# Performance work log

Measured on AMD Instinct MI355X. Metric: run time of the kernel, lower is better.

The kernel has to match this reference:

```python
import jax, jax.numpy as jnp
import numpy as np

B, T, D = 1, 1024, 1024
H, KVH, HD = 16, 4, 64          # heads, kv heads, head dim (D = H*HD)
E, K, FF = 8, 2, 2048           # experts, top_k, expert hidden
CF, ROPE_THETA, CLIP = 2.0, 500000.0, 8.0
CAP = int(np.ceil(B * T * K * CF / E))  # per-expert capacity (=512)
EPS = 1e-5


def layernorm(x, w):
    mu = jnp.mean(x, -1, keepdims=True)
    var = jnp.var(x, -1, keepdims=True)
    return (x - mu) * jax.lax.rsqrt(var + EPS) * w


def rotate_half(u):
    u1, u2 = u[..., : HD // 2], u[..., HD // 2 :]
    return jnp.concatenate([-u2, u1], axis=-1)


def rope(q, k, position_ids):
    inv_freq = 1.0 / (ROPE_THETA ** (jnp.arange(0, HD, 2, dtype=jnp.float32) / HD))
    ang = position_ids.astype(jnp.float32)[..., None] * inv_freq  # (B,T,HD/2)
    emb = jnp.concatenate([ang, ang], axis=-1)                    # (B,T,HD)
    cos = jnp.cos(emb)[:, :, None, :]  # broadcast over heads -> (B,T,1,HD)
    sin = jnp.sin(emb)[:, :, None, :]
    q = q * cos + rotate_half(q) * sin
    k = k * cos + rotate_half(k) * sin
    return q, k


def setup_inputs() -> dict:
    key = jax.random.key(0)
    ks = jax.random.split(key, 12)
    s = 0.02
    return {
        "hidden_states": jax.random.normal(ks[0], (B, T, D), jnp.float32),
        "position_ids": jnp.tile(jnp.arange(T, dtype=jnp.int32)[None, :], (B, 1)),
        "ln1_w": jnp.ones((D,), jnp.float32),
        "ln2_w": jnp.ones((D,), jnp.float32),
        "Wq": jax.random.normal(ks[1], (D, H * HD), jnp.float32) * s,
        "Wk": jax.random.normal(ks[2], (D, KVH * HD), jnp.float32) * s,
        "Wv": jax.random.normal(ks[3], (D, KVH * HD), jnp.float32) * s,
        "Wo": jax.random.normal(ks[4], (H * HD, D), jnp.float32) * s,
        "Wr": jax.random.normal(ks[5], (D, E), jnp.float32) * s,
        "Wg": jax.random.normal(ks[6], (E, D, FF), jnp.float32) * s,
        "Wu": jax.random.normal(ks[7], (E, D, FF), jnp.float32) * s,
        "Wd": jax.random.normal(ks[8], (E, FF, D), jnp.float32) * s,
    }


def reference(hidden_states, position_ids, ln1_w, ln2_w, Wq, Wk, Wv, Wo, Wr, Wg, Wu, Wd):
    x = hidden_states
    # ---- attention (pre-LN, clip_qkv, RoPE, GQA, causal) ----
    res = x
    h = layernorm(x, ln1_w)
    q = jnp.clip(h @ Wq, -CLIP, CLIP).reshape(B, T, H, HD)
    k = jnp.clip(h @ Wk, -CLIP, CLIP).reshape(B, T, KVH, HD)
    v = jnp.clip(h @ Wv, -CLIP, CLIP).reshape(B, T, KVH, HD)
    q, k = rope(q, k, position_ids)
    k = jnp.repeat(k, H // KVH, axis=2)  # GQA expand -> (B,T,H,HD)
    v = jnp.repeat(v, H // KVH, axis=2)
    scores = jnp.einsum("bthd,bshd->bhts", q, k) / jnp.sqrt(jnp.float32(HD))
    causal = jnp.tril(jnp.ones((T, T), bool))
    scores = jnp.where(causal[None, None], scores, jnp.finfo(scores.dtype).min)
    attn = jax.nn.softmax(scores, axis=-1)
    o = jnp.einsum("bhts,bshd->bthd", attn, v).reshape(B, T, H * HD) @ Wo
    x = res + o
    # ---- MoE FFN (top-k router, capacity-based dispatch, GLU experts) ----
    res = x
    h = layernorm(x, ln2_w).reshape(B * T, D)
    N = B * T
    probs = jax.nn.softmax(h @ Wr, axis=-1)            # (N,E)
    vals, idx = jax.lax.top_k(probs, K)                # (N,K)
    gate = vals / jnp.sum(vals, -1, keepdims=True)     # normalize_top_k_affinities
    e_flat = idx.reshape(-1)                           # (N*K,)
    g_flat = gate.reshape(-1)
    tok = jnp.repeat(jnp.arange(N), K)                 # source token per assignment
    oh = jax.nn.one_hot(e_flat, E, dtype=jnp.int32)
    pos = jnp.cumsum(oh, axis=0)[jnp.arange(N * K), e_flat] - 1  # slot within expert
    keep = pos < CAP                                   # capacity drop mask
    slot = jnp.where(keep, pos, CAP)                   # overflow -> trash slot
    xb = jnp.zeros((E, CAP + 1, D), h.dtype).at[e_flat, slot].set(h[tok])
    act = jax.nn.silu(jnp.einsum("ecd,edf->ecf", xb, Wg)) * jnp.einsum("ecd,edf->ecf", xb, Wu)
    ob = jnp.einsum("ecf,efd->ecd", act, Wd)           # (E,CAP+1,D)
    contrib = ob[e_flat, slot] * (g_flat * keep.astype(h.dtype))[:, None]
    y = jnp.zeros((N, D), h.dtype).at[tok].add(contrib).reshape(B, T, D)
    return res + y
```

## Files before the change

kernel.cpp:

```cpp
#include <hip/hip_runtime.h>
#include <math.h>

typedef __attribute__((ext_vector_type(8))) short bfrag;
typedef __attribute__((ext_vector_type(8))) unsigned short u16x8;
typedef __attribute__((ext_vector_type(4))) float f32x4;

__device__ __forceinline__ unsigned short bf16_rne(float f) {
  unsigned int u = __float_as_uint(f);
  u += 0x7FFFu + ((u >> 16) & 1u);
  return (unsigned short)(u >> 16);
}
__device__ __forceinline__ float bf16f(unsigned short h) {
  return __uint_as_float(((unsigned int)h) << 16);
}
__device__ __forceinline__ void split3(float x, unsigned short &o1, unsigned short &o2, unsigned short &o3) {
  o1 = bf16_rne(x);
  const float r1 = x - bf16f(o1);
  o2 = bf16_rne(r1);
  const float r2 = r1 - bf16f(o2);
  o3 = bf16_rne(r2);
}
__device__ __forceinline__ void split2(float x, unsigned short &o1, unsigned short &o2) {
  o1 = bf16_rne(x);
  o2 = bf16_rne(x - bf16f(o1));
}

__global__ __launch_bounds__(256) void ln_kernel(const float* __restrict__ x,
                                                 const float* __restrict__ w,
                                                 float* __restrict__ out) {
  const int t = blockIdx.x;
  const int tid = threadIdx.x;
  const float4 v = *reinterpret_cast<const float4*>(&x[(size_t)t * 1024 + tid * 4]);
  float s = v.x + v.y + v.z + v.w;
  float ss = v.x * v.x + v.y * v.y + v.z * v.z + v.w * v.w;
#pragma unroll
  for (int off = 32; off; off >>= 1) {
    s += __shfl_xor(s, off);
    ss += __shfl_xor(ss, off);
  }
  __shared__ float red1[4], red2[4];
  if ((tid & 63) == 0) { red1[tid >> 6] = s; red2[tid >> 6] = ss; }
  __syncthreads();
  s = red1[0] + red1[1] + red1[2] + red1[3];
  ss = red2[0] + red2[1] + red2[2] + red2[3];
  const float mu = s * (1.0f / 1024.0f);
  const float var = ss * (1.0f / 1024.0f) - mu * mu;
  const float rstd = 1.0f / sqrtf(var + 1e-5f);
  const float4 wv = *reinterpret_cast<const float4*>(&w[tid * 4]);
  float4 o;
  o.x = (v.x - mu) * rstd * wv.x;
  o.y = (v.y - mu) * rstd * wv.y;
  o.z = (v.z - mu) * rstd * wv.z;
  o.w = (v.w - mu) * rstd * wv.w;
  *reinterpret_cast<float4*>(&out[(size_t)t * 1024 + tid * 4]) = o;
}

__global__ __launch_bounds__(256) void ln_split3_kernel(
    const float* __restrict__ x, const float* __restrict__ w,
    unsigned short* __restrict__ d1, unsigned short* __restrict__ d2,
    unsigned short* __restrict__ d3) {
  const int t = blockIdx.x;
  const int tid = threadIdx.x;
  const float4 v = *reinterpret_cast<const float4*>(&x[(size_t)t * 1024 + tid * 4]);
  float s = v.x + v.y + v.z + v.w;
  float ss = v.x * v.x + v.y * v.y + v.z * v.z + v.w * v.w;
#pragma unroll
  for (int off = 32; off; off >>= 1) {
    s += __shfl_xor(s, off);
    ss += __shfl_xor(ss, off);
  }
  __shared__ float red1[4], red2[4];
  if ((tid & 63) == 0) { red1[tid >> 6] = s; red2[tid >> 6] = ss; }
  __syncthreads();
  s = red1[0] + red1[1] + red1[2] + red1[3];
  ss = red2[0] + red2[1] + red2[2] + red2[3];
  const float mu = s * (1.0f / 1024.0f);
  const float var = ss * (1.0f / 1024.0f) - mu * mu;
  const float rstd = 1.0f / sqrtf(var + 1e-5f);
  const float4 wv = *reinterpret_cast<const float4*>(&w[tid * 4]);
  float4 o;
  o.x = (v.x - mu) * rstd * wv.x;
  o.y = (v.y - mu) * rstd * wv.y;
  o.z = (v.z - mu) * rstd * wv.z;
  o.w = (v.w - mu) * rstd * wv.w;
  ushort4 a, b, c;
  split3(o.x, a.x, b.x, c.x);
  split3(o.y, a.y, b.y, c.y);
  split3(o.z, a.z, b.z, c.z);
  split3(o.w, a.w, b.w, c.w);
  const int i = t * 256 + tid;
  reinterpret_cast<ushort4*>(d1)[i] = a;
  reinterpret_cast<ushort4*>(d2)[i] = b;
  reinterpret_cast<ushort4*>(d3)[i] = c;
}

__global__ __launch_bounds__(256) void split3t_kernel(
    const float* __restrict__ src, unsigned short* __restrict__ d1,
    unsigned short* __restrict__ d2, unsigned short* __restrict__ d3,
    int K, int N) {
  __shared__ float tile[32][33];
  const int k0 = blockIdx.x * 32, n0 = blockIdx.y * 32;
  const int tx = threadIdx.x & 31, ty = threadIdx.x >> 5;
#pragma unroll
  for (int i = 0; i < 4; ++i)
    tile[ty + i * 8][tx] = src[(size_t)(k0 + ty + i * 8) * N + n0 + tx];
  __syncthreads();
#pragma unroll
  for (int i = 0; i < 4; ++i) {
    const float v = tile[tx][ty + i * 8];
    unsigned short s1, s2, s3;
    split3(v, s1, s2, s3);
    const size_t o = (size_t)(n0 + ty + i * 8) * K + k0 + tx;
    d1[o] = s1; d2[o] = s2; d3[o] = s3;
  }
}

__device__ __forceinline__ void gemm_ps_body(
    const unsigned short* __restrict__ A1, const unsigned short* __restrict__ A2,
    const unsigned short* __restrict__ A3, const unsigned short* __restrict__ B1,
    const unsigned short* __restrict__ B2, const unsigned short* __restrict__ B3,
    float* __restrict__ C, const float* __restrict__ Res,
    int N, int K, int doclip, int m0, int n0) {
  __shared__ alignas(16) unsigned short As[3][32][40];
  __shared__ alignas(16) unsigned short Bs[3][64][40];
  const int tid = threadIdx.x;
  const int w = tid >> 6, l = tid & 63;
  const int wm = (w & 1) * 16, wn = (w >> 1) * 32;
  const int lr = l & 15, lg = l >> 4;
  const int arow = tid >> 3, aslot = tid & 7;

  const unsigned short* Ap[3] = {A1, A2, A3};
  const unsigned short* Bp[3] = {B1, B2, B3};

  f32x4 acc[2] = {{0.f,0.f,0.f,0.f},{0.f,0.f,0.f,0.f}};

  for (int k0 = 0; k0 < K; k0 += 32) {
#pragma unroll
    for (int s = 0; s < 3; ++s) {
      *reinterpret_cast<ushort4*>(&As[s][arow][aslot * 4]) =
          *reinterpret_cast<const ushort4*>(&Ap[s][(size_t)(m0 + arow) * K + k0 + aslot * 4]);
#pragma unroll
      for (int p = 0; p < 2; ++p) {
        const int row = arow + p * 32;
        *reinterpret_cast<ushort4*>(&Bs[s][row][aslot * 4]) =
            *reinterpret_cast<const ushort4*>(&Bp[s][(size_t)(n0 + row) * K + k0 + aslot * 4]);
      }
    }
    __syncthreads();
    bfrag af[3], bg[2][3];
#pragma unroll
    for (int s = 0; s < 3; ++s)
      af[s] = *reinterpret_cast<const bfrag*>(&As[s][wm + lr][lg * 8]);
#pragma unroll
    for (int ni = 0; ni < 2; ++ni)
#pragma unroll
      for (int s = 0; s < 3; ++s)
        bg[ni][s] = *reinterpret_cast<const bfrag*>(&Bs[s][wn + ni * 16 + lr][lg * 8]);
#pragma unroll
    for (int ni = 0; ni < 2; ++ni) {
      f32x4 c = acc[ni];
      c = __builtin_amdgcn_mfma_f32_16x16x32_bf16(af[2], bg[ni][0], c, 0, 0, 0);
      c = __builtin_amdgcn_mfma_f32_16x16x32_bf16(af[1], bg[ni][1], c, 0, 0, 0);
      c = __builtin_amdgcn_mfma_f32_16x16x32_bf16(af[0], bg[ni][2], c, 0, 0, 0);
      c = __builtin_amdgcn_mfma_f32_16x16x32_bf16(af[1], bg[ni][0], c, 0, 0, 0);
      c = __builtin_amdgcn_mfma_f32_16x16x32_bf16(af[0], bg[ni][1], c, 0, 0, 0);
      c = __builtin_amdgcn_mfma_f32_16x16x32_bf16(af[0], bg[ni][0], c, 0, 0, 0);
      acc[ni] = c;
    }
    __syncthreads();
  }
#pragma unroll
  for (int ni = 0; ni < 2; ++ni)
#pragma unroll
    for (int r = 0; r < 4; ++r) {
      const int row = m0 + wm + lg * 4 + r;
      const int col = n0 + wn + ni * 16 + lr;
      float vv = acc[ni][r];
      if (doclip) vv = fminf(fmaxf(vv, -8.0f), 8.0f);
      if (Res) vv += Res[(size_t)row * N + col];
      C[(size_t)row * N + col] = vv;
    }
}

__global__ __launch_bounds__(256) void gemm_ps_kernel(
    const unsigned short* __restrict__ A1, const unsigned short* __restrict__ A2,
    const unsigned short* __restrict__ A3, const unsigned short* __restrict__ B1,
    const unsigned short* __restrict__ B2, const unsigned short* __restrict__ B3,
    float* __restrict__ C, const float* __restrict__ Res,
    int N, int K, int doclip) {
  gemm_ps_body(A1, A2, A3, B1, B2, B3, C, Res, N, K, doclip,
               blockIdx.x * 32, blockIdx.y * 64);
}

__global__ __launch_bounds__(256) void gemm_qkv_kernel(
    const unsigned short* __restrict__ A1, const unsigned short* __restrict__ A2,
    const unsigned short* __restrict__ A3,
    const unsigned short* __restrict__ Q1, const unsigned short* __restrict__ Q2,
    const unsigned short* __restrict__ Q3,
    const unsigned short* __restrict__ K1, const unsigned short* __restrict__ K2,
    const unsigned short* __restrict__ K3,
    const unsigned short* __restrict__ V1, const unsigned short* __restrict__ V2,
    const unsigned short* __restrict__ V3,
    float* __restrict__ qb, float* __restrict__ kb, float* __restrict__ vb) {
  const int by = blockIdx.y;
  const unsigned short *B1, *B2, *B3;
  float* C;
  int N, n0;
  if (by < 16)      { B1 = Q1; B2 = Q2; B3 = Q3; C = qb; N = 1024; n0 = by * 64; }
  else if (by < 20) { B1 = K1; B2 = K2; B3 = K3; C = kb; N = 256;  n0 = (by - 16) * 64; }
  else              { B1 = V1; B2 = V2; B3 = V3; C = vb; N = 256;  n0 = (by - 20) * 64; }
  gemm_ps_body(A1, A2, A3, B1, B2, B3, C, nullptr, N, 1024, 1, blockIdx.x * 32, n0);
}

__global__ void rope_table_kernel(const int* __restrict__ posids,
                                  float* __restrict__ cosT, float* __restrict__ sinT) {
  const int t = blockIdx.x * 8 + (threadIdx.x >> 5);
  const int i = threadIdx.x & 31;
  const double ang = (double)posids[t] * pow(500000.0, -(double)i / 32.0);
  cosT[t * 32 + i] = (float)cos(ang);
  sinT[t * 32 + i] = (float)sin(ang);
}

__global__ void rope_kernel(float* __restrict__ q, float* __restrict__ k,
                            const float* __restrict__ cosT, const float* __restrict__ sinT) {
  const int t = blockIdx.x;
  const int hh = blockIdx.y;
  const int i = threadIdx.x;
  float* ptr = (hh < 16) ? &q[((size_t)t * 16 + hh) * 64]
                         : &k[((size_t)t * 4 + (hh - 16)) * 64];
  const float c = cosT[t * 32 + i], s = sinT[t * 32 + i];
  const float u1 = ptr[i], u2 = ptr[i + 32];
  ptr[i]      = u1 * c - u2 * s;
  ptr[i + 32] = u2 * c + u1 * s;
}

__global__ __launch_bounds__(256) void prep_kv_kernel(
    const float* __restrict__ k, const float* __restrict__ v,
    unsigned short* __restrict__ Kp1, unsigned short* __restrict__ Kp2,
    unsigned short* __restrict__ Vp1, unsigned short* __restrict__ Vp2) {
  const int key = blockIdx.x;
  const int kvh = threadIdx.x >> 6;
  const int d = threadIdx.x & 63;
  const float kk = k[((size_t)key * 4 + kvh) * 64 + d];
  const float vv = v[((size_t)key * 4 + kvh) * 64 + d];
  unsigned short a1, a2, b1, b2;
  split2(kk, a1, a2);
  split2(vv, b1, b2);
  const size_t ki = ((size_t)kvh * 1024 + key) * 64 + d;
  Kp1[ki] = a1; Kp2[ki] = a2;
  const size_t vi = ((size_t)kvh * 64 + d) * 1024 + key;
  Vp1[vi] = b1; Vp2[vi] = b2;
}

__global__ __launch_bounds__(256) void attn_kernel(
    const float* __restrict__ q,
    const unsigned short* __restrict__ Kp1, const unsigned short* __restrict__ Kp2,
    const unsigned short* __restrict__ Vp1, const unsigned short* __restrict__ Vp2,
    unsigned short* __restrict__ o1, unsigned short* __restrict__ o2,
    unsigned short* __restrict__ o3) {
  const int qt = blockIdx.x, h = blockIdx.y, kvh = h >> 2;
  __shared__ unsigned short Ks1[64][72], Ks2[64][72], Vt1[64][72], Vt2[64][72];
  __shared__ unsigned short Ps1[4][16][72], Ps2[4][16][72];
  const int tid = threadIdx.x;
  const int w = tid >> 6, l = tid & 63;
  const int lr = l & 15, lg = l >> 4;

  bfrag aq1[2], aq2[2];
  {
    const int tq = qt * 64 + w * 16 + lr;
    const float* qrow = &q[((size_t)tq * 16 + h) * 64];
#pragma unroll
    for (int ks = 0; ks < 2; ++ks) {
      const int d0 = ks * 32 + lg * 8;
      const float4 f0 = *reinterpret_cast<const float4*>(qrow + d0);
      const float4 f1 = *reinterpret_cast<const float4*>(qrow + d0 + 4);
      const float xv[8] = {f0.x, f0.y, f0.z, f0.w, f1.x, f1.y, f1.z, f1.w};
#pragma unroll
      for (int j = 0; j < 8; ++j) {
        const float xs = xv[j] * 0.125f;
        unsigned short p1, p2;
        split2(xs, p1, p2);
        aq1[ks][j] = (short)p1;
        aq2[ks][j] = (short)p2;
      }
    }
  }

  f32x4 accO[4] = {{0.f,0.f,0.f,0.f},{0.f,0.f,0.f,0.f},{0.f,0.f,0.f,0.f},{0.f,0.f,0.f,0.f}};
  float mrun[4] = {-INFINITY, -INFINITY, -INFINITY, -INFINITY};
  float lrun[4] = {0.f, 0.f, 0.f, 0.f};

  for (int ti = 0; ti <= qt; ++ti) {
    const int s0 = ti * 64;
    {
      const size_t kbase = ((size_t)kvh * 1024 + s0 + l) * 64 + w * 16;
      *reinterpret_cast<u16x8*>(&Ks1[l][w * 16])     = *reinterpret_cast<const u16x8*>(&Kp1[kbase]);
      *reinterpret_cast<u16x8*>(&Ks1[l][w * 16 + 8]) = *reinterpret_cast<const u16x8*>(&Kp1[kbase + 8]);
      *reinterpret_cast<u16x8*>(&Ks2[l][w * 16])     = *reinterpret_cast<const u16x8*>(&Kp2[kbase]);
      *reinterpret_cast<u16x8*>(&Ks2[l][w * 16 + 8]) = *reinterpret_cast<const u16x8*>(&Kp2[kbase + 8]);
      const size_t vbase = ((size_t)kvh * 64 + l) * 1024 + s0 + w * 16;
      *reinterpret_cast<u16x8*>(&Vt1[l][w * 16])     = *reinterpret_cast<const u16x8*>(&Vp1[vbase]);
      *reinterpret_cast<u16x8*>(&Vt1[l][w * 16 + 8]) = *reinterpret_cast<const u16x8*>(&Vp1[vbase + 8]);
      *reinterpret_cast<u16x8*>(&Vt2[l][w * 16])     = *reinterpret_cast<const u16x8*>(&Vp2[vbase]);
      *reinterpret_cast<u16x8*>(&Vt2[l][w * 16 + 8]) = *reinterpret_cast<const u16x8*>(&Vp2[vbase + 8]);
    }
    __syncthreads();

    f32x4 accS[4] = {{0.f,0.f,0.f,0.f},{0.f,0.f,0.f,0.f},{0.f,0.f,0.f,0.f},{0.f,0.f,0.f,0.f}};
#pragma unroll
    for (int ks = 0; ks < 2; ++ks) {
      const int koff = ks * 32 + lg * 8;
#pragma unroll
      for (int ni = 0; ni < 4; ++ni) {
        const bfrag b1 = *reinterpret_cast<const bfrag*>(&Ks1[ni * 16 + lr][koff]);
        const bfrag b2 = *reinterpret_cast<const bfrag*>(&Ks2[ni * 16 + lr][koff]);
        f32x4 c = accS[ni];
        c = __builtin_amdgcn_mfma_f32_16x16x32_bf16(aq1[ks], b2, c, 0, 0, 0);
        c = __builtin_amdgcn_mfma_f32_16x16x32_bf16(aq2[ks], b1, c, 0, 0, 0);
        c = __builtin_amdgcn_mfma_f32_16x16x32_bf16(aq1[ks], b1, c, 0, 0, 0);
        accS[ni] = c;
      }
    }
    if (ti == qt) {
      const int rowb = w * 16 + lg * 4;
#pragma unroll
      for (int ni = 0; ni < 4; ++ni)
#pragma unroll
        for (int r = 0; r < 4; ++r)
          if (ni * 16 + lr > rowb + r) accS[ni][r] = -INFINITY;
    }
    float alpha[4];
#pragma unroll
    for (int r = 0; r < 4; ++r) {
      float tm = fmaxf(fmaxf(accS[0][r], accS[1][r]), fmaxf(accS[2][r], accS[3][r]));
      tm = fmaxf(tm, __shfl_xor(tm, 1));
      tm = fmaxf(tm, __shfl_xor(tm, 2));
      tm = fmaxf(tm, __shfl_xor(tm, 4));
      tm = fmaxf(tm, __shfl_xor(tm, 8));
      const float mnew = fmaxf(mrun[r], tm);
      alpha[r] = __expf(mrun[r] - mnew);
      mrun[r] = mnew;
      float ps = 0.f;
#pragma unroll
      for (int ni = 0; ni < 4; ++ni) {
        const float pv = __expf(accS[ni][r] - mnew);
        accS[ni][r] = pv;
        ps += pv;
      }
      ps += __shfl_xor(ps, 1);
      ps += __shfl_xor(ps, 2);
      ps += __shfl_xor(ps, 4);
      ps += __shfl_xor(ps, 8);
      lrun[r] = lrun[r] * alpha[r] + ps;
    }
#pragma unroll
    for (int ni = 0; ni < 4; ++ni)
#pragma unroll
      for (int r = 0; r < 4; ++r) {
        const float pv = accS[ni][r];
        unsigned short p1, p2;
        split2(pv, p1, p2);
        Ps1[w][lg * 4 + r][ni * 16 + lr] = p1;
        Ps2[w][lg * 4 + r][ni * 16 + lr] = p2;
      }
#pragma unroll
    for (int ni = 0; ni < 4; ++ni)
#pragma unroll
      for (int r = 0; r < 4; ++r) accO[ni][r] *= alpha[r];

    asm volatile("s_waitcnt lgkmcnt(0)" ::: "memory");

#pragma unroll
    for (int kk = 0; kk < 2; ++kk) {
      const int koff = kk * 32 + lg * 8;
      const bfrag pa1 = *reinterpret_cast<const bfrag*>(&Ps1[w][lr][koff]);
      const bfrag pa2 = *reinterpret_cast<const bfrag*>(&Ps2[w][lr][koff]);
#pragma unroll
      for (int ni = 0; ni < 4; ++ni) {
        const bfrag vb1 = *reinterpret_cast<const bfrag*>(&Vt1[ni * 16 + lr][koff]);
        const bfrag vb2 = *reinterpret_cast<const bfrag*>(&Vt2[ni * 16 + lr][koff]);
        f32x4 c = accO[ni];
        c = __builtin_amdgcn_mfma_f32_16x16x32_bf16(pa1, vb2, c, 0, 0, 0);
        c = __builtin_amdgcn_mfma_f32_16x16x32_bf16(pa2, vb1, c, 0, 0, 0);
        c = __builtin_amdgcn_mfma_f32_16x16x32_bf16(pa1, vb1, c, 0, 0, 0);
        accO[ni] = c;
      }
    }
    __syncthreads();
  }

  const int tqo = qt * 64 + w * 16 + lg * 4;
#pragma unroll
  for (int r = 0; r < 4; ++r) {
    const float inv = 1.0f / lrun[r];
#pragma unroll
    for (int ni = 0; ni < 4; ++ni) {
      const size_t oi = (size_t)(tqo + r) * 1024 + h * 64 + ni * 16 + lr;
      unsigned short s1, s2, s3;
      split3(accO[ni][r] * inv, s1, s2, s3);
      o1[oi] = s1; o2[oi] = s2; o3[oi] = s3;
    }
  }
}

__global__ __launch_bounds__(64) void router_kernel(const float* __restrict__ h2,
                                                    const float* __restrict__ Wr,
                                                    int* __restrict__ eidx,
                                                    float* __restrict__ egate) {
  const int t = blockIdx.x;
  const int l = threadIdx.x;
  float p[8];
#pragma unroll
  for (int e = 0; e < 8; ++e) p[e] = 0.f;
  for (int d = l; d < 1024; d += 64) {
    const float x = h2[(size_t)t * 1024 + d];
    const float4 w0 = *reinterpret_cast<const float4*>(&Wr[d * 8]);
    const float4 w1 = *reinterpret_cast<const float4*>(&Wr[d * 8 + 4]);
    p[0] += x * w0.x; p[1] += x * w0.y; p[2] += x * w0.z; p[3] += x * w0.w;
    p[4] += x * w1.x; p[5] += x * w1.y; p[6] += x * w1.z; p[7] += x * w1.w;
  }
#pragma unroll
  for (int off = 32; off; off >>= 1) {
#pragma unroll
    for (int e = 0; e < 8; ++e) p[e] += __shfl_xor(p[e], off);
  }
  if (l == 0) {
    int i0 = 0; float b0 = p[0];
#pragma unroll
    for (int e = 1; e < 8; ++e) if (p[e] > b0) { b0 = p[e]; i0 = e; }
    int i1 = -1; float b1 = -INFINITY;
#pragma unroll
    for (int e = 0; e < 8; ++e) if (e != i0 && p[e] > b1) { b1 = p[e]; i1 = e; }
    const float ex = expf(b1 - b0);
    eidx[t * 2] = i0; eidx[t * 2 + 1] = i1;
    egate[t * 2] = 1.0f / (1.0f + ex);
    egate[t * 2 + 1] = ex / (1.0f + ex);
  }
}

__global__ __launch_bounds__(256) void dispatch_kernel(
    const int* __restrict__ eidx, int* __restrict__ cnt,
    int* __restrict__ slot_token, int* __restrict__ entry_slot) {
  __shared__ unsigned char ef[2048];
  __shared__ unsigned short ch[256][8];
  const int tid = threadIdx.x;
  for (int i = tid; i < 2048; i += 256) ef[i] = (unsigned char)eidx[i];
  __syncthreads();
  int loc[8];
#pragma unroll
  for (int e = 0; e < 8; ++e) loc[e] = 0;
  const int base = tid * 8;
  for (int j = 0; j < 8; ++j) {
    const int ee = ef[base + j];
#pragma unroll
    for (int e = 0; e < 8; ++e) loc[e] += (ee == e);
  }
#pragma unroll
  for (int e = 0; e < 8; ++e) ch[tid][e] = (unsigned short)loc[e];
  __syncthreads();
  int pre[8];
#pragma unroll
  for (int e = 0; e < 8; ++e) pre[e] = 0;
  for (int t2 = 0; t2 < tid; ++t2) {
#pragma unroll
    for (int e = 0; e < 8; ++e) pre[e] += ch[t2][e];
  }
  if (tid == 255) {
#pragma unroll
    for (int e = 0; e < 8; ++e) cnt[e] = min(pre[e] + loc[e], 512);
  }
  for (int j = 0; j < 8; ++j) {
    const int i = base + j;
    const int ee = ef[i];
    int slot = 0;
#pragma unroll
    for (int e = 0; e < 8; ++e) {
      if (e == ee) { slot = pre[e]; pre[e] = pre[e] + 1; }
    }
    if (slot < 512) {
      slot_token[ee * 512 + slot] = i >> 1;
      entry_slot[i] = slot;
    } else {
      entry_slot[i] = -1;
    }
  }
}

__global__ __launch_bounds__(256) void moe_xbf_kernel(
    const float* __restrict__ h2, const int* __restrict__ cnt,
    const int* __restrict__ slot_token, unsigned short* __restrict__ xbf) {
  const int row = blockIdx.x;
  const int e = row >> 9, slot = row & 511;
  const int tid = threadIdx.x;
  ushort4 o;
  if (slot < cnt[e]) {
    const int tok = slot_token[row];
    const float4 f = *reinterpret_cast<const float4*>(&h2[(size_t)tok * 1024 + tid * 4]);
    o = make_ushort4(bf16_rne(f.x), bf16_rne(f.y), bf16_rne(f.z), bf16_rne(f.w));
  } else {
    o = make_ushort4(0, 0, 0, 0);
  }
  *reinterpret_cast<ushort4*>(&xbf[(size_t)row * 1024 + tid * 4]) = o;
}

__global__ __launch_bounds__(256, 2) void moe_mlp1_kernel(
    const unsigned short* __restrict__ xbf, const float* __restrict__ Wg,
    const float* __restrict__ Wu, const int* __restrict__ cnt,
    unsigned short* __restrict__ act) {
  const int bx = blockIdx.x;
  const int e = bx & 7, nt = bx >> 3;
  const int n0 = nt * 32;
  const int ce = cnt[e];
  if (ce <= 0) return;
  __shared__ alignas(16) unsigned short BgL[2][32][72], BuL[2][32][72];
  const int tid = threadIdx.x;
  const int w = tid >> 6, l = tid & 63;
  const int lr = l & 15, lg = l >> 4;
  const int wc = tid & 31, kq8 = tid >> 5;
  const float* WgE = Wg + (size_t)e * 1024 * 2048 + (size_t)kq8 * 8 * 2048 + n0 + wc;
  const float* WuE = Wu + (size_t)e * 1024 * 2048 + (size_t)kq8 * 8 * 2048 + n0 + wc;
  const unsigned short* xbE = xbf + (size_t)e * 512 * 1024;

  f32x4 accG[8][2], accU[8][2];
#pragma unroll
  for (int mi = 0; mi < 8; ++mi)
#pragma unroll
    for (int ni = 0; ni < 2; ++ni) {
      accG[mi][ni] = (f32x4){0.f, 0.f, 0.f, 0.f};
      accU[mi][ni] = (f32x4){0.f, 0.f, 0.f, 0.f};
    }

  float wgr[8], wur[8];
#pragma unroll
  for (int j = 0; j < 8; ++j) { wgr[j] = WgE[(size_t)j * 2048]; wur[j] = WuE[(size_t)j * 2048]; }
  {
    u16x8 g8, u8;
#pragma unroll
    for (int j = 0; j < 8; ++j) { g8[j] = bf16_rne(wgr[j]); u8[j] = bf16_rne(wur[j]); }
    *reinterpret_cast<u16x8*>(&BgL[0][wc][kq8 * 8]) = g8;
    *reinterpret_cast<u16x8*>(&BuL[0][wc][kq8 * 8]) = u8;
  }
#pragma unroll
  for (int j = 0; j < 8; ++j) { wgr[j] = WgE[(size_t)(64 + j) * 2048]; wur[j] = WuE[(size_t)(64 + j) * 2048]; }
  __syncthreads();

  for (int t = 0; t < 16; ++t) {
    const int cur = t & 1;
    bfrag bgf[2][2], buf2[2][2];
#pragma unroll
    for (int ni = 0; ni < 2; ++ni)
#pragma unroll
      for (int kf = 0; kf < 2; ++kf) {
        bgf[ni][kf]  = *reinterpret_cast<const bfrag*>(&BgL[cur][ni * 16 + lr][kf * 32 + lg * 8]);
        buf2[ni][kf] = *reinterpret_cast<const bfrag*>(&BuL[cur][ni * 16 + lr][kf * 32 + lg * 8]);
      }
    u16x8 g8, u8;
    if (t < 15) {
#pragma unroll
      for (int j = 0; j < 8; ++j) { g8[j] = bf16_rne(wgr[j]); u8[j] = bf16_rne(wur[j]); }
    }
    if (t < 14) {
      const size_t kb = (size_t)(t + 2) * 64;
#pragma unroll
      for (int j = 0; j < 8; ++j) { wgr[j] = WgE[(kb + j) * 2048]; wur[j] = WuE[(kb + j) * 2048]; }
    }
    const int kA = t * 64 + lg * 8;
#pragma unroll
    for (int mi = 0; mi < 8; ++mi) {
      const int row0 = (mi * 4 + w) * 16;
      if (row0 < ce) {
        const unsigned short* ap = &xbE[(size_t)(row0 + lr) * 1024 + kA];
        const bfrag a0 = *reinterpret_cast<const bfrag*>(ap);
        const bfrag a1 = *reinterpret_cast<const bfrag*>(ap + 32);
#pragma unroll
        for (int ni = 0; ni < 2; ++ni) {
          accG[mi][ni] = __builtin_amdgcn_mfma_f32_16x16x32_bf16(a0, bgf[ni][0], accG[mi][ni], 0, 0, 0);
          accG[mi][ni] = __builtin_amdgcn_mfma_f32_16x16x32_bf16(a1, bgf[ni][1], accG[mi][ni], 0, 0, 0);
          accU[mi][ni] = __builtin_amdgcn_mfma_f32_16x16x32_bf16(a0, buf2[ni][0], accU[mi][ni], 0, 0, 0);
          accU[mi][ni] = __builtin_amdgcn_mfma_f32_16x16x32_bf16(a1, buf2[ni][1], accU[mi][ni], 0, 0, 0);
        }
      }
    }
    if (t < 15) {
      *reinterpret_cast<u16x8*>(&BgL[cur ^ 1][wc][kq8 * 8]) = g8;
      *reinterpret_cast<u16x8*>(&BuL[cur ^ 1][wc][kq8 * 8]) = u8;
    }
    __syncthreads();
  }
#pragma unroll
  for (int mi = 0; mi < 8; ++mi) {
    const int row0 = (mi * 4 + w) * 16;
    if (row0 < ce) {
#pragma unroll
      for (int r = 0; r < 4; ++r) {
        const int m = row0 + lg * 4 + r;
        if (m < ce) {
#pragma unroll
          for (int ni = 0; ni < 2; ++ni) {
            const float gg = accG[mi][ni][r];
            const float uu = accU[mi][ni][r];
            const float a = gg / (1.0f + __expf(-gg)) * uu;
            act[((size_t)e * 512 + m) * 2048 + n0 + ni * 16 + lr] = bf16_rne(a);
          }
        }
      }
    }
  }
}

__global__ __launch_bounds__(256, 2) void moe_mlp2_kernel(
    const unsigned short* __restrict__ act, const float* __restrict__ Wd,
    const int* __restrict__ cnt, float* __restrict__ ob) {
  const int bx = blockIdx.x;
  const int e = bx & 7;
  const int rr = bx >> 3;
  const int nt = rr & 31, kc = rr >> 5;
  const int n0 = nt * 32;
  const int ce = cnt[e];
  if (ce <= 0) return;
  __shared__ alignas(16) unsigned short BsL[2][32][72];
  const int tid = threadIdx.x;
  const int w = tid >> 6, l = tid & 63;
  const int lr = l & 15, lg = l >> 4;
  const int wc = tid & 31, kq8 = tid >> 5;
  const unsigned short* actE = act + (size_t)e * 512 * 2048 + (size_t)kc * 1024;
  const float* WdE = Wd + (size_t)e * 2048 * 1024 + (size_t)(kc * 1024 + kq8 * 8) * 1024 + n0 + wc;
  float* obE = ob + (size_t)kc * 8 * 512 * 1024;

  f32x4 acc[8][2];
#pragma unroll
  for (int mi = 0; mi < 8; ++mi)
#pragma unroll
    for (int ni = 0; ni < 2; ++ni) acc[mi][ni] = (f32x4){0.f, 0.f, 0.f, 0.f};

  float wdr[8];
#pragma unroll
  for (int j = 0; j < 8; ++j) wdr[j] = WdE[(size_t)j * 1024];
  {
    u16x8 d8;
#pragma unroll
    for (int j = 0; j < 8; ++j) d8[j] = bf16_rne(wdr[j]);
    *reinterpret_cast<u16x8*>(&BsL[0][wc][kq8 * 8]) = d8;
  }
#pragma unroll
  for (int j = 0; j < 8; ++j) wdr[j] = WdE[(size_t)(64 + j) * 1024];
  __syncthreads();

  for (int t = 0; t < 16; ++t) {
    const int cur = t & 1;
    bfrag bf2[2][2];
#pragma unroll
    for (int ni = 0; ni < 2; ++ni)
#pragma unroll
      for (int kf = 0; kf < 2; ++kf)
        bf2[ni][kf] = *reinterpret_cast<const bfrag*>(&BsL[cur][ni * 16 + lr][kf * 32 + lg * 8]);
    u16x8 d8;
    if (t < 15) {
#pragma unroll
      for (int j = 0; j < 8; ++j) d8[j] = bf16_rne(wdr[j]);
    }
    if (t < 14) {
      const size_t kb = (size_t)(t + 2) * 64;
#pragma unroll
      for (int j = 0; j < 8; ++j) wdr[j] = WdE[(kb + j) * 1024];
    }
    const int kA = t * 64 + lg * 8;
#pragma unroll
    for (int mi = 0; mi < 8; ++mi) {
      const int row0 = (mi * 4 + w) * 16;
      if (row0 < ce) {
        const unsigned short* ap = &actE[(size_t)(row0 + lr) * 2048 + kA];
        const bfrag a0 = *reinterpret_cast<const bfrag*>(ap);
        const bfrag a1 = *reinterpret_cast<const bfrag*>(ap + 32);
#pragma unroll
        for (int ni = 0; ni < 2; ++ni) {
          acc[mi][ni] = __builtin_amdgcn_mfma_f32_16x16x32_bf16(a0, bf2[ni][0], acc[mi][ni], 0, 0, 0);
          acc[mi][ni] = __builtin_amdgcn_mfma_f32_16x16x32_bf16(a1, bf2[ni][1], acc[mi][ni], 0, 0, 0);
        }
      }
    }
    if (t < 15) {
      *reinterpret_cast<u16x8*>(&BsL[cur ^ 1][wc][kq8 * 8]) = d8;
    }
    __syncthreads();
  }
#pragma unroll
  for (int mi = 0; mi < 8; ++mi) {
    const int row0 = (mi * 4 + w) * 16;
    if (row0 < ce) {
#pragma unroll
      for (int r = 0; r < 4; ++r) {
        const int m = row0 + lg * 4 + r;
        if (m < ce) {
#pragma unroll
          for (int ni = 0; ni < 2; ++ni)
            obE[((size_t)e * 512 + m) * 1024 + n0 + ni * 16 + lr] = acc[mi][ni][r];
        }
      }
    }
  }
}

__global__ __launch_bounds__(256) void combine_kernel(
    const float* __restrict__ ob, const int* __restrict__ eidx,
    const float* __restrict__ egate, const int* __restrict__ entry_slot,
    float* __restrict__ out) {
  const int t = blockIdx.x;
  const int d = threadIdx.x * 4;
  const size_t half = (size_t)8 * 512 * 1024;
  float4 o4 = *reinterpret_cast<float4*>(&out[(size_t)t * 1024 + d]);
#pragma unroll
  for (int kk = 0; kk < 2; ++kk) {
    const int i = t * 2 + kk;
    const int s = entry_slot[i];
    if (s >= 0) {
      const int e = eidx[i];
      const float g = egate[i];
      const size_t base = ((size_t)e * 512 + s) * 1024 + d;
      const float4 c0 = *reinterpret_cast<const float4*>(&ob[base]);
      const float4 c1 = *reinterpret_cast<const float4*>(&ob[half + base]);
      o4.x += g * (c0.x + c1.x); o4.y += g * (c0.y + c1.y);
      o4.z += g * (c0.z + c1.z); o4.w += g * (c0.w + c1.w);
    }
  }
  *reinterpret_cast<float4*>(&out[(size_t)t * 1024 + d]) = o4;
}

extern "C" void kernel_launch(void* const* d_in, const int* in_sizes, int n_in,
                              void* d_out, int out_size, void* d_ws, size_t ws_size,
                              hipStream_t stream) {
  const float* hidden = (const float*)d_in[0];
  const int* posids  = (const int*)d_in[1];
  const float* ln1w  = (const float*)d_in[2];
  const float* ln2w  = (const float*)d_in[3];
  const float* Wq    = (const float*)d_in[4];
  const float* Wk    = (const float*)d_in[5];
  const float* Wv    = (const float*)d_in[6];
  const float* Wo    = (const float*)d_in[7];
  const float* Wr    = (const float*)d_in[8];
  const float* Wg    = (const float*)d_in[9];
  const float* Wu    = (const float*)d_in[10];
  const float* Wd    = (const float*)d_in[11];
  float* out = (float*)d_out;

  char* p = (char*)d_ws;
  auto alloc = [&](size_t bytes) { char* r = p; p += (bytes + 255) & ~(size_t)255; return r; };
  float* qb   = (float*)alloc((size_t)1024 * 1024 * 4);
  float* kb   = (float*)alloc((size_t)1024 * 256 * 4);
  float* vb   = (float*)alloc((size_t)1024 * 256 * 4);
  float* h2   = (float*)alloc((size_t)1024 * 1024 * 4);
  unsigned short* act = (unsigned short*)alloc((size_t)8 * 512 * 2048 * 2);
  float* obuf = (float*)alloc((size_t)2 * 8 * 512 * 1024 * 4);
  int* eidx   = (int*)alloc(2048 * 4);
  float* egate = (float*)alloc(2048 * 4);
  int* cnt    = (int*)alloc(8 * 4);
  int* slot_token = (int*)alloc((size_t)8 * 512 * 4);
  int* entry_slot = (int*)alloc(2048 * 4);
  float* cosT = (float*)alloc((size_t)1024 * 32 * 4);
  float* sinT = (float*)alloc((size_t)1024 * 32 * 4);
  unsigned short* Kp1 = (unsigned short*)alloc((size_t)4 * 1024 * 64 * 2);
  unsigned short* Kp2 = (unsigned short*)alloc((size_t)4 * 1024 * 64 * 2);
  unsigned short* Vp1 = (unsigned short*)alloc((size_t)4 * 1024 * 64 * 2);
  unsigned short* Vp2 = (unsigned short*)alloc((size_t)4 * 1024 * 64 * 2);
  unsigned short* xbf = (unsigned short*)alloc((size_t)8 * 512 * 1024 * 2);
  const size_t MK = (size_t)1024 * 1024;
  unsigned short* h1s[3], *aos[3], *wqt[3], *wkt[3], *wvt[3], *wot[3];
  for (int s = 0; s < 3; ++s) h1s[s] = (unsigned short*)alloc(MK * 2);
  for (int s = 0; s < 3; ++s) aos[s] = (unsigned short*)alloc(MK * 2);
  for (int s = 0; s < 3; ++s) wqt[s] = (unsigned short*)alloc(MK * 2);
  for (int s = 0; s < 3; ++s) wkt[s] = (unsigned short*)alloc((size_t)256 * 1024 * 2);
  for (int s = 0; s < 3; ++s) wvt[s] = (unsigned short*)alloc((size_t)256 * 1024 * 2);
  for (int s = 0; s < 3; ++s) wot[s] = (unsigned short*)alloc(MK * 2);

  rope_table_kernel<<<128, 256, 0, stream>>>(posids, cosT, sinT);
  split3t_kernel<<<dim3(32, 32), 256, 0, stream>>>(Wq, wqt[0], wqt[1], wqt[2], 1024, 1024);
  split3t_kernel<<<dim3(32, 8),  256, 0, stream>>>(Wk, wkt[0], wkt[1], wkt[2], 1024, 256);
  split3t_kernel<<<dim3(32, 8),  256, 0, stream>>>(Wv, wvt[0], wvt[1], wvt[2], 1024, 256);
  split3t_kernel<<<dim3(32, 32), 256, 0, stream>>>(Wo, wot[0], wot[1], wot[2], 1024, 1024);

  ln_split3_kernel<<<1024, 256, 0, stream>>>(hidden, ln1w, h1s[0], h1s[1], h1s[2]);
  gemm_qkv_kernel<<<dim3(32, 24), 256, 0, stream>>>(h1s[0], h1s[1], h1s[2],
      wqt[0], wqt[1], wqt[2], wkt[0], wkt[1], wkt[2], wvt[0], wvt[1], wvt[2],
      qb, kb, vb);
  rope_kernel<<<dim3(1024, 20), 32, 0, stream>>>(qb, kb, cosT, sinT);
  prep_kv_kernel<<<1024, 256, 0, stream>>>(kb, vb, Kp1, Kp2, Vp1, Vp2);
  attn_kernel<<<dim3(16, 16), 256, 0, stream>>>(qb, Kp1, Kp2, Vp1, Vp2,
      aos[0], aos[1], aos[2]);
  gemm_ps_kernel<<<dim3(32, 16), 256, 0, stream>>>(aos[0], aos[1], aos[2],
      wot[0], wot[1], wot[2], out, hidden, 1024, 1024, 0);
  ln_kernel<<<1024, 256, 0, stream>>>(out, ln2w, h2);
  router_kernel<<<1024, 64, 0, stream>>>(h2, Wr, eidx, egate);
  dispatch_kernel<<<1, 256, 0, stream>>>(eidx, cnt, slot_token, entry_slot);
  moe_xbf_kernel<<<4096, 256, 0, stream>>>(h2, cnt, slot_token, xbf);
  moe_mlp1_kernel<<<512, 256, 0, stream>>>(xbf, Wg, Wu, cnt, act);
  moe_mlp2_kernel<<<512, 256, 0, stream>>>(act, Wd, cnt, obuf);
  combine_kernel<<<1024, 256, 0, stream>>>(obuf, eidx, egate, entry_slot, out);
}
```

Before: 312.0 us.

## Fuse RoPE into KV prep and attention, merge weight splits, enlarge GEMM tiles

Result: faster. 305.5 us (-2.1%).

```diff
diff --git a/kernel.cpp b/kernel.cpp
--- a/kernel.cpp
+++ b/kernel.cpp
@@ -94,12 +94,24 @@
   reinterpret_cast<ushort4*>(d3)[i] = c;
 }
 
-__global__ __launch_bounds__(256) void split3t_kernel(
-    const float* __restrict__ src, unsigned short* __restrict__ d1,
-    unsigned short* __restrict__ d2, unsigned short* __restrict__ d3,
-    int K, int N) {
+__global__ __launch_bounds__(256) void split3t_all_kernel(
+    const float* __restrict__ Wq, const float* __restrict__ Wk,
+    const float* __restrict__ Wv, const float* __restrict__ Wo,
+    unsigned short* __restrict__ q1, unsigned short* __restrict__ q2, unsigned short* __restrict__ q3,
+    unsigned short* __restrict__ k1, unsigned short* __restrict__ k2, unsigned short* __restrict__ k3,
+    unsigned short* __restrict__ v1, unsigned short* __restrict__ v2, unsigned short* __restrict__ v3,
+    unsigned short* __restrict__ o1, unsigned short* __restrict__ o2, unsigned short* __restrict__ o3) {
   __shared__ float tile[32][33];
-  const int k0 = blockIdx.x * 32, n0 = blockIdx.y * 32;
+  const int bid = blockIdx.x;
+  const float* src;
+  unsigned short *d1, *d2, *d3;
+  int N, local;
+  if (bid < 1024)      { src = Wq; d1 = q1; d2 = q2; d3 = q3; N = 1024; local = bid; }
+  else if (bid < 1280) { src = Wk; d1 = k1; d2 = k2; d3 = k3; N = 256;  local = bid - 1024; }
+  else if (bid < 1536) { src = Wv; d1 = v1; d2 = v2; d3 = v3; N = 256;  local = bid - 1280; }
+  else                 { src = Wo; d1 = o1; d2 = o2; d3 = o3; N = 1024; local = bid - 1536; }
+  const int K = 1024;
+  const int k0 = (local & 31) * 32, n0 = (local >> 5) * 32;
   const int tx = threadIdx.x & 31, ty = threadIdx.x >> 5;
 #pragma unroll
   for (int i = 0; i < 4; ++i)
@@ -115,71 +127,74 @@
   }
 }
 
-__device__ __forceinline__ void gemm_ps_body(
+__device__ __forceinline__ void gemm64_body(
     const unsigned short* __restrict__ A1, const unsigned short* __restrict__ A2,
     const unsigned short* __restrict__ A3, const unsigned short* __restrict__ B1,
     const unsigned short* __restrict__ B2, const unsigned short* __restrict__ B3,
     float* __restrict__ C, const float* __restrict__ Res,
     int N, int K, int doclip, int m0, int n0) {
-  __shared__ alignas(16) unsigned short As[3][32][40];
+  __shared__ alignas(16) unsigned short As[3][64][40];
   __shared__ alignas(16) unsigned short Bs[3][64][40];
   const int tid = threadIdx.x;
   const int w = tid >> 6, l = tid & 63;
-  const int wm = (w & 1) * 16, wn = (w >> 1) * 32;
+  const int wm = (w >> 1) * 32, wn = (w & 1) * 32;
   const int lr = l & 15, lg = l >> 4;
-  const int arow = tid >> 3, aslot = tid & 7;
+  const int arow = tid >> 2, kslot = tid & 3;
 
   const unsigned short* Ap[3] = {A1, A2, A3};
   const unsigned short* Bp[3] = {B1, B2, B3};
 
-  f32x4 acc[2] = {{0.f,0.f,0.f,0.f},{0.f,0.f,0.f,0.f}};
+  f32x4 acc[2][2] = {{{0.f,0.f,0.f,0.f},{0.f,0.f,0.f,0.f}},
+                     {{0.f,0.f,0.f,0.f},{0.f,0.f,0.f,0.f}}};
 
   for (int k0 = 0; k0 < K; k0 += 32) {
 #pragma unroll
     for (int s = 0; s < 3; ++s) {
-      *reinterpret_cast<ushort4*>(&As[s][arow][aslot * 4]) =
-          *reinterpret_cast<const ushort4*>(&Ap[s][(size_t)(m0 + arow) * K + k0 + aslot * 4]);
-#pragma unroll
-      for (int p = 0; p < 2; ++p) {
-        const int row = arow + p * 32;
-        *reinterpret_cast<ushort4*>(&Bs[s][row][aslot * 4]) =
-            *reinterpret_cast<const ushort4*>(&Bp[s][(size_t)(n0 + row) * K + k0 + aslot * 4]);
-      }
+      *reinterpret_cast<u16x8*>(&As[s][arow][kslot * 8]) =
+          *reinterpret_cast<const u16x8*>(&Ap[s][(size_t)(m0 + arow) * K + k0 + kslot * 8]);
+      *reinterpret_cast<u16x8*>(&Bs[s][arow][kslot * 8]) =
+          *reinterpret_cast<const u16x8*>(&Bp[s][(size_t)(n0 + arow) * K + k0 + kslot * 8]);
     }
     __syncthreads();
-    bfrag af[3], bg[2][3];
-#pragma unroll
-    for (int s = 0; s < 3; ++s)
-      af[s] = *reinterpret_cast<const bfrag*>(&As[s][wm + lr][lg * 8]);
+    bfrag af[2][3], bg[2][3];
+#pragma unroll
+    for (int mi = 0; mi < 2; ++mi)
+#pragma unroll
+      for (int s = 0; s < 3; ++s)
+        af[mi][s] = *reinterpret_cast<const bfrag*>(&As[s][wm + mi * 16 + lr][lg * 8]);
 #pragma unroll
     for (int ni = 0; ni < 2; ++ni)
 #pragma unroll
       for (int s = 0; s < 3; ++s)
         bg[ni][s] = *reinterpret_cast<const bfrag*>(&Bs[s][wn + ni * 16 + lr][lg * 8]);
 #pragma unroll
-    for (int ni = 0; ni < 2; ++ni) {
-      f32x4 c = acc[ni];
-      c = __builtin_amdgcn_mfma_f32_16x16x32_bf16(af[2], bg[ni][0], c, 0, 0, 0);
-      c = __builtin_amdgcn_mfma_f32_16x16x32_bf16(af[1], bg[ni][1], c, 0, 0, 0);
-      c = __builtin_amdgcn_mfma_f32_16x16x32_bf16(af[0], bg[ni][2], c, 0, 0, 0);
-      c = __builtin_amdgcn_mfma_f32_16x16x32_bf16(af[1], bg[ni][0], c, 0, 0, 0);
-      c = __builtin_amdgcn_mfma_f32_16x16x32_bf16(af[0], bg[ni][1], c, 0, 0, 0);
-      c = __builtin_amdgcn_mfma_f32_16x16x32_bf16(af[0], bg[ni][0], c, 0, 0, 0);
-      acc[ni] = c;
-    }
+    for (int mi = 0; mi < 2; ++mi)
+#pragma unroll
+      for (int ni = 0; ni < 2; ++ni) {
+        f32x4 c = acc[mi][ni];
+        c = __builtin_amdgcn_mfma_f32_16x16x32_bf16(af[mi][2], bg[ni][0], c, 0, 0, 0);
+        c = __builtin_amdgcn_mfma_f32_16x16x32_bf16(af[mi][1], bg[ni][1], c, 0, 0, 0);
+        c = __builtin_amdgcn_mfma_f32_16x16x32_bf16(af[mi][0], bg[ni][2], c, 0, 0, 0);
+        c = __builtin_amdgcn_mfma_f32_16x16x32_bf16(af[mi][1], bg[ni][0], c, 0, 0, 0);
+        c = __builtin_amdgcn_mfma_f32_16x16x32_bf16(af[mi][0], bg[ni][1], c, 0, 0, 0);
+        c = __builtin_amdgcn_mfma_f32_16x16x32_bf16(af[mi][0], bg[ni][0], c, 0, 0, 0);
+        acc[mi][ni] = c;
+      }
     __syncthreads();
   }
 #pragma unroll
-  for (int ni = 0; ni < 2; ++ni)
-#pragma unroll
-    for (int r = 0; r < 4; ++r) {
-      const int row = m0 + wm + lg * 4 + r;
-      const int col = n0 + wn + ni * 16 + lr;
-      float vv = acc[ni][r];
-      if (doclip) vv = fminf(fmaxf(vv, -8.0f), 8.0f);
-      if (Res) vv += Res[(size_t)row * N + col];
-      C[(size_t)row * N + col] = vv;
-    }
+  for (int mi = 0; mi < 2; ++mi)
+#pragma unroll
+    for (int ni = 0; ni < 2; ++ni)
+#pragma unroll
+      for (int r = 0; r < 4; ++r) {
+        const int row = m0 + wm + mi * 16 + lg * 4 + r;
+        const int col = n0 + wn + ni * 16 + lr;
+        float vv = acc[mi][ni][r];
+        if (doclip) vv = fminf(fmaxf(vv, -8.0f), 8.0f);
+        if (Res) vv += Res[(size_t)row * N + col];
+        C[(size_t)row * N + col] = vv;
+      }
 }
 
 __global__ __launch_bounds__(256) void gemm_ps_kernel(
@@ -188,8 +203,8 @@
     const unsigned short* __restrict__ B2, const unsigned short* __restrict__ B3,
     float* __restrict__ C, const float* __restrict__ Res,
     int N, int K, int doclip) {
-  gemm_ps_body(A1, A2, A3, B1, B2, B3, C, Res, N, K, doclip,
-               blockIdx.x * 32, blockIdx.y * 64);
+  gemm64_body(A1, A2, A3, B1, B2, B3, C, Res, N, K, doclip,
+              blockIdx.x * 64, blockIdx.y * 64);
 }
 
 __global__ __launch_bounds__(256) void gemm_qkv_kernel(
@@ -209,7 +224,7 @@
   if (by < 16)      { B1 = Q1; B2 = Q2; B3 = Q3; C = qb; N = 1024; n0 = by * 64; }
   else if (by < 20) { B1 = K1; B2 = K2; B3 = K3; C = kb; N = 256;  n0 = (by - 16) * 64; }
   else              { B1 = V1; B2 = V2; B3 = V3; C = vb; N = 256;  n0 = (by - 20) * 64; }
-  gemm_ps_body(A1, A2, A3, B1, B2, B3, C, nullptr, N, 1024, 1, blockIdx.x * 32, n0);
+  gemm64_body(A1, A2, A3, B1, B2, B3, C, nullptr, N, 1024, 1, blockIdx.x * 64, n0);
 }
 
 __global__ void rope_table_kernel(const int* __restrict__ posids,
@@ -221,27 +236,19 @@
   sinT[t * 32 + i] = (float)sin(ang);
 }
 
-__global__ void rope_kernel(float* __restrict__ q, float* __restrict__ k,
-                            const float* __restrict__ cosT, const float* __restrict__ sinT) {
-  const int t = blockIdx.x;
-  const int hh = blockIdx.y;
-  const int i = threadIdx.x;
-  float* ptr = (hh < 16) ? &q[((size_t)t * 16 + hh) * 64]
-                         : &k[((size_t)t * 4 + (hh - 16)) * 64];
-  const float c = cosT[t * 32 + i], s = sinT[t * 32 + i];
-  const float u1 = ptr[i], u2 = ptr[i + 32];
-  ptr[i]      = u1 * c - u2 * s;
-  ptr[i + 32] = u2 * c + u1 * s;
-}
-
 __global__ __launch_bounds__(256) void prep_kv_kernel(
     const float* __restrict__ k, const float* __restrict__ v,
+    const float* __restrict__ cosT, const float* __restrict__ sinT,
     unsigned short* __restrict__ Kp1, unsigned short* __restrict__ Kp2,
     unsigned short* __restrict__ Vp1, unsigned short* __restrict__ Vp2) {
   const int key = blockIdx.x;
   const int kvh = threadIdx.x >> 6;
   const int d = threadIdx.x & 63;
-  const float kk = k[((size_t)key * 4 + kvh) * 64 + d];
+  const int dd = d & 31;
+  const float* kbase = &k[((size_t)key * 4 + kvh) * 64];
+  const float c = cosT[key * 32 + dd], s = sinT[key * 32 + dd];
+  const float u1 = kbase[dd], u2 = kbase[dd + 32];
+  const float kk = (d < 32) ? (u1 * c - u2 * s) : (u2 * c + u1 * s);
   const float vv = v[((size_t)key * 4 + kvh) * 64 + d];
   unsigned short a1, a2, b1, b2;
   split2(kk, a1, a2);
@@ -254,6 +261,7 @@
 
 __global__ __launch_bounds__(256) void attn_kernel(
     const float* __restrict__ q,
+    const float* __restrict__ cosT, const float* __restrict__ sinT,
     const unsigned short* __restrict__ Kp1, const unsigned short* __restrict__ Kp2,
     const unsigned short* __restrict__ Vp1, const unsigned short* __restrict__ Vp2,
     unsigned short* __restrict__ o1, unsigned short* __restrict__ o2,
@@ -269,20 +277,23 @@
   {
     const int tq = qt * 64 + w * 16 + lr;
     const float* qrow = &q[((size_t)tq * 16 + h) * 64];
-#pragma unroll
-    for (int ks = 0; ks < 2; ++ks) {
-      const int d0 = ks * 32 + lg * 8;
-      const float4 f0 = *reinterpret_cast<const float4*>(qrow + d0);
-      const float4 f1 = *reinterpret_cast<const float4*>(qrow + d0 + 4);
-      const float xv[8] = {f0.x, f0.y, f0.z, f0.w, f1.x, f1.y, f1.z, f1.w};
-#pragma unroll
-      for (int j = 0; j < 8; ++j) {
-        const float xs = xv[j] * 0.125f;
-        unsigned short p1, p2;
-        split2(xs, p1, p2);
-        aq1[ks][j] = (short)p1;
-        aq2[ks][j] = (short)p2;
-      }
+    const float4 f00 = *reinterpret_cast<const float4*>(qrow + lg * 8);
+    const float4 f01 = *reinterpret_cast<const float4*>(qrow + lg * 8 + 4);
+    const float4 f10 = *reinterpret_cast<const float4*>(qrow + 32 + lg * 8);
+    const float4 f11 = *reinterpret_cast<const float4*>(qrow + 32 + lg * 8 + 4);
+    const float x0[8] = {f00.x, f00.y, f00.z, f00.w, f01.x, f01.y, f01.z, f01.w};
+    const float x1[8] = {f10.x, f10.y, f10.z, f10.w, f11.x, f11.y, f11.z, f11.w};
+#pragma unroll
+    for (int j = 0; j < 8; ++j) {
+      const float c = cosT[tq * 32 + lg * 8 + j];
+      const float s = sinT[tq * 32 + lg * 8 + j];
+      const float r0 = x0[j] * c - x1[j] * s;
+      const float r1 = x1[j] * c + x0[j] * s;
+      unsigned short p1, p2;
+      split2(r0 * 0.125f, p1, p2);
+      aq1[0][j] = (short)p1; aq2[0][j] = (short)p2;
+      split2(r1 * 0.125f, p1, p2);
+      aq1[1][j] = (short)p1; aq2[1][j] = (short)p2;
     }
   }
 
@@ -773,20 +784,18 @@
   for (int s = 0; s < 3; ++s) wot[s] = (unsigned short*)alloc(MK * 2);
 
   rope_table_kernel<<<128, 256, 0, stream>>>(posids, cosT, sinT);
-  split3t_kernel<<<dim3(32, 32), 256, 0, stream>>>(Wq, wqt[0], wqt[1], wqt[2], 1024, 1024);
-  split3t_kernel<<<dim3(32, 8),  256, 0, stream>>>(Wk, wkt[0], wkt[1], wkt[2], 1024, 256);
-  split3t_kernel<<<dim3(32, 8),  256, 0, stream>>>(Wv, wvt[0], wvt[1], wvt[2], 1024, 256);
-  split3t_kernel<<<dim3(32, 32), 256, 0, stream>>>(Wo, wot[0], wot[1], wot[2], 1024, 1024);
+  split3t_all_kernel<<<2560, 256, 0, stream>>>(Wq, Wk, Wv, Wo,
+      wqt[0], wqt[1], wqt[2], wkt[0], wkt[1], wkt[2],
+      wvt[0], wvt[1], wvt[2], wot[0], wot[1], wot[2]);
 
   ln_split3_kernel<<<1024, 256, 0, stream>>>(hidden, ln1w, h1s[0], h1s[1], h1s[2]);
-  gemm_qkv_kernel<<<dim3(32, 24), 256, 0, stream>>>(h1s[0], h1s[1], h1s[2],
+  gemm_qkv_kernel<<<dim3(16, 24), 256, 0, stream>>>(h1s[0], h1s[1], h1s[2],
       wqt[0], wqt[1], wqt[2], wkt[0], wkt[1], wkt[2], wvt[0], wvt[1], wvt[2],
       qb, kb, vb);
-  rope_kernel<<<dim3(1024, 20), 32, 0, stream>>>(qb, kb, cosT, sinT);
-  prep_kv_kernel<<<1024, 256, 0, stream>>>(kb, vb, Kp1, Kp2, Vp1, Vp2);
-  attn_kernel<<<dim3(16, 16), 256, 0, stream>>>(qb, Kp1, Kp2, Vp1, Vp2,
+  prep_kv_kernel<<<1024, 256, 0, stream>>>(kb, vb, cosT, sinT, Kp1, Kp2, Vp1, Vp2);
+  attn_kernel<<<dim3(16, 16), 256, 0, stream>>>(qb, cosT, sinT, Kp1, Kp2, Vp1, Vp2,
       aos[0], aos[1], aos[2]);
-  gemm_ps_kernel<<<dim3(32, 16), 256, 0, stream>>>(aos[0], aos[1], aos[2],
+  gemm_ps_kernel<<<dim3(16, 16), 256, 0, stream>>>(aos[0], aos[1], aos[2],
       wot[0], wot[1], wot[2], out, hidden, 1024, 1024, 0);
   ln_kernel<<<1024, 256, 0, stream>>>(out, ln2w, h2);
   router_kernel<<<1024, 64, 0, stream>>>(h2, Wr, eidx, egate);
```
